# Optimization experiments

Hardware: AMD Instinct MI355X
Metric: run time of the kernel (lower is better)

Reference implementation:

```python
import jax, jax.numpy as jnp
import numpy as np

N_NODES = 100000
N_EDGES = 1600000
HIDDEN = 64


def setup_inputs() -> dict:
    key = jax.random.key(0)
    ks = jax.random.split(key, 10)
    s = 0.1
    x = jax.random.normal(ks[0], (N_NODES, 1), dtype=jnp.float32)
    edge_index = jax.random.randint(ks[1], (2, N_EDGES), 0, N_NODES, dtype=jnp.int32)
    edge_weight = jnp.ones((N_EDGES,), dtype=jnp.float32)
    f32 = jnp.float32
    return {
        "x": x,
        "edge_weight": edge_weight,
        "Wz": jax.random.normal(ks[2], (1, HIDDEN), f32) * s,
        "bz": jnp.zeros((HIDDEN,), f32),
        "Lz": jax.random.normal(ks[3], (2 * HIDDEN, HIDDEN), f32) * s,
        "lbz": jnp.zeros((HIDDEN,), f32),
        "Wr": jax.random.normal(ks[4], (1, HIDDEN), f32) * s,
        "br": jnp.zeros((HIDDEN,), f32),
        "Lr": jax.random.normal(ks[5], (2 * HIDDEN, HIDDEN), f32) * s,
        "lbr": jnp.zeros((HIDDEN,), f32),
        "Wh": jax.random.normal(ks[6], (1, HIDDEN), f32) * s,
        "bh": jnp.zeros((HIDDEN,), f32),
        "Lh": jax.random.normal(ks[7], (2 * HIDDEN, HIDDEN), f32) * s,
        "lbh": jnp.zeros((HIDDEN,), f32),
        "Wout": jax.random.normal(ks[8], (HIDDEN, 1), f32) * s,
        "bout": jnp.zeros((1,), f32),
        "edge_index": edge_index,
    }


def reference(x, edge_weight, Wz, bz, Lz, lbz, Wr, br, Lr, lbr,
              Wh, bh, Lh, lbh, Wout, bout, edge_index):
    N = x.shape[0]
    hidden = Wz.shape[1]
    src, dst = edge_index[0], edge_index[1]
    # GCN normalization with added self-loops (PyG gcn_norm)
    loop = jnp.arange(N, dtype=src.dtype)
    src2 = jnp.concatenate([src, loop])
    dst2 = jnp.concatenate([dst, loop])
    ew2 = jnp.concatenate([edge_weight, jnp.ones((N,), x.dtype)])
    deg = jax.ops.segment_sum(ew2, dst2, num_segments=N)  # [N]
    dinv = jnp.where(deg > 0, jax.lax.rsqrt(deg), 0.0)
    norm = dinv[src2] * ew2 * dinv[dst2]  # [E+N]

    def gcn(W, b):
        xw = x @ W  # [N, H]
        agg = jax.ops.segment_sum(xw[src2] * norm[:, None], dst2, num_segments=N)
        return agg + b

    # TGCN cell with H0 = 0 (no hidden state passed)
    H = jnp.zeros((N, hidden), x.dtype)
    Z = jax.nn.sigmoid(jnp.concatenate([gcn(Wz, bz), H], axis=1) @ Lz + lbz)
    R = jax.nn.sigmoid(jnp.concatenate([gcn(Wr, br), H], axis=1) @ Lr + lbr)
    Ht = jnp.tanh(jnp.concatenate([gcn(Wh, bh), H * R], axis=1) @ Lh + lbh)
    Hn = Z * H + (1.0 - Z) * Ht
    h = jax.nn.relu(Hn)
    return h @ Wout + bout
```

## Files before the change

kernel.cpp:

```cpp
#include <hip/hip_runtime.h>
#include <math.h>

#define HIDDEN 64
#define RANGE 16384
#define RSHIFT 14
#define G 32
#define PACK_SHIFT 17

__device__ __forceinline__ void map_rc(int b, int nranges, int& r, int& c) {
    int x = b & 7;
    int rest = b >> 3;
    r = rest % nranges;
    c = x + 8 * (rest / nranges);
}

__global__ __launch_bounds__(1024)
void k_binA(const int* __restrict__ dst, const int* __restrict__ src,
            const float* __restrict__ ew, float* __restrict__ partials,
            uint2* __restrict__ comp, int* __restrict__ counts,
            int N, int E, int nranges, int cap) {
    __shared__ float bins[RANGE];
    __shared__ int cursor;
    float4* b4 = (float4*)bins;
    for (int i = threadIdx.x; i < RANGE / 4; i += blockDim.x)
        b4[i] = make_float4(0.f, 0.f, 0.f, 0.f);
    if (threadIdx.x == 0) cursor = 0;
    __syncthreads();

    int r, c;
    map_rc(blockIdx.x, nranges, r, c);
    const int base = r * RANGE;
    const unsigned rsize = (unsigned)min(RANGE, N - base);
    uint2* slice = comp + (size_t)(r * G + c) * cap;

    long long e0 = (((long long)E * c) / G) & ~3LL;
    long long e1 = (c == G - 1) ? (long long)E
                                : ((((long long)E * (c + 1)) / G) & ~3LL);
    const int nvec = (int)((e1 - e0) >> 2);
    const int4*   dst4 = (const int4*)(dst + e0);
    const int4*   src4 = (const int4*)(src + e0);
    const float4* ew4  = (const float4*)(ew + e0);
    const int lane = threadIdx.x & 63;

    for (int i = threadIdx.x; i < nvec; i += blockDim.x) {
        int4   d = dst4[i];
        int4   s = src4[i];
        float4 t = ew4[i];
        int   dd[4] = {d.x, d.y, d.z, d.w};
        int   ss[4] = {s.x, s.y, s.z, s.w};
        float tt[4] = {t.x, t.y, t.z, t.w};
        #pragma unroll
        for (int j = 0; j < 4; ++j) {
            unsigned l = (unsigned)(dd[j] - base);
            bool p = l < rsize;
            if (p) atomicAdd(&bins[l], tt[j]);
            unsigned long long m = __ballot(p);
            if (m) {
                int leader = __ffsll((unsigned long long)m) - 1;
                int pre = __popcll(m & ((1ULL << lane) - 1ULL));
                int bpos = 0;
                if (lane == leader) bpos = atomicAdd(&cursor, __popcll(m));
                bpos = __shfl(bpos, leader);
                if (p) slice[bpos + pre] =
                    make_uint2((l << PACK_SHIFT) | (unsigned)ss[j],
                               __float_as_uint(tt[j]));
            }
        }
    }
    for (long long e = e0 + ((long long)nvec << 2) + threadIdx.x; e < e1; e += blockDim.x) {
        unsigned l = (unsigned)(dst[e] - base);
        if (l < rsize) {
            atomicAdd(&bins[l], ew[e]);
            int bpos = atomicAdd(&cursor, 1);
            slice[bpos] = make_uint2((l << PACK_SHIFT) | (unsigned)src[e],
                                     __float_as_uint(ew[e]));
        }
    }
    __syncthreads();

    float4* outp = (float4*)(partials + ((size_t)c * nranges + r) * RANGE);
    for (int i = threadIdx.x; i < RANGE / 4; i += blockDim.x) outp[i] = b4[i];
    if (threadIdx.x == 0) counts[r * G + c] = cursor;
}

__global__ void k_node(const float* __restrict__ x, const float* __restrict__ partials,
                       float* __restrict__ dinv, float* __restrict__ w,
                       int N, int nranges,
                       const float* __restrict__ Wz, const float* __restrict__ bz,
                       const float* __restrict__ Lz, const float* __restrict__ lbz,
                       const float* __restrict__ Wh, const float* __restrict__ bh,
                       const float* __restrict__ Lh, const float* __restrict__ lbh,
                       float* __restrict__ coeff) {
    int i = blockIdx.x * blockDim.x + threadIdx.x;
    if (i < N) {
        int r = i >> RSHIFT, local = i & (RANGE - 1);
        const float* p = partials + (size_t)r * RANGE + local;
        float d = 1.0f;
        #pragma unroll
        for (int c = 0; c < G; ++c) d += p[(size_t)c * nranges * RANGE];
        float di = rsqrtf(d);
        dinv[i] = di;
        w[i] = di * x[i];
    }
    if (blockIdx.x == 0 && threadIdx.x < HIDDEN) {
        int j = threadIdx.x;
        float vz = 0.f, cz = 0.f, vh = 0.f, ch = 0.f;
        for (int k = 0; k < HIDDEN; ++k) {
            float lz = Lz[k * HIDDEN + j];
            float lh = Lh[k * HIDDEN + j];
            vz += Wz[k] * lz;
            cz += bz[k] * lz;
            vh += Wh[k] * lh;
            ch += bh[k] * lh;
        }
        coeff[j]       = vz;
        coeff[64 + j]  = cz + lbz[j];
        coeff[128 + j] = vh;
        coeff[192 + j] = ch + lbh[j];
    }
}

__global__ __launch_bounds__(1024)
void k_binB(const uint2* __restrict__ comp, const int* __restrict__ counts,
            const float* __restrict__ w, float* __restrict__ partials,
            int nranges, int cap) {
    __shared__ float bins[RANGE];
    float4* b4 = (float4*)bins;
    for (int i = threadIdx.x; i < RANGE / 4; i += blockDim.x)
        b4[i] = make_float4(0.f, 0.f, 0.f, 0.f);
    __syncthreads();

    int r, c;
    map_rc(blockIdx.x, nranges, r, c);
    const uint2* slice = comp + (size_t)(r * G + c) * cap;
    const int n = counts[r * G + c];

    for (int i = threadIdx.x; i < n; i += blockDim.x) {
        uint2 e = slice[i];
        float v = w[e.x & ((1u << PACK_SHIFT) - 1u)] * __uint_as_float(e.y);
        atomicAdd(&bins[e.x >> PACK_SHIFT], v);
    }
    __syncthreads();

    float4* outp = (float4*)(partials + ((size_t)c * nranges + r) * RANGE);
    for (int i = threadIdx.x; i < RANGE / 4; i += blockDim.x) outp[i] = b4[i];
}

__global__ void k_out(const float* __restrict__ partials, const float* __restrict__ dinv,
                      const float* __restrict__ w, const float* __restrict__ coeff,
                      const float* __restrict__ Wout, const float* __restrict__ bout,
                      float* __restrict__ out, int N, int nranges) {
    __shared__ float c[5 * HIDDEN];
    __shared__ float b0;
    if (threadIdx.x < 4 * HIDDEN) c[threadIdx.x] = coeff[threadIdx.x];
    if (threadIdx.x < HIDDEN) c[4 * HIDDEN + threadIdx.x] = Wout[threadIdx.x];
    if (threadIdx.x == 0) b0 = bout[0];
    __syncthreads();
    int i = blockIdx.x * blockDim.x + threadIdx.x;
    if (i < N) {
        int r = i >> RSHIFT, local = i & (RANGE - 1);
        const float* p = partials + (size_t)r * RANGE + local;
        float g = w[i];
        #pragma unroll
        for (int k = 0; k < G; ++k) g += p[(size_t)k * nranges * RANGE];
        float si = dinv[i] * g;
        float acc = b0;
        #pragma unroll
        for (int j = 0; j < HIDDEN; ++j) {
            float zp = fminf(fmaxf(si * c[j] + c[64 + j], -30.f), 30.f);
            float hp = fminf(fmaxf(si * c[128 + j] + c[192 + j], -15.f), 15.f);
            float a  = __expf(2.0f * hp);
            float t  = (a - 1.0f) / (a + 1.0f);
            float zn = 1.0f / (1.0f + __expf(zp));
            float hn = zn * t;
            hn = hn > 0.0f ? hn : 0.0f;
            acc = fmaf(hn, c[256 + j], acc);
        }
        out[i] = acc;
    }
}

extern "C" void kernel_launch(void* const* d_in, const int* in_sizes, int n_in,
                              void* d_out, int out_size, void* d_ws, size_t ws_size,
                              hipStream_t stream) {
    const float* x    = (const float*)d_in[0];
    const float* ew   = (const float*)d_in[1];
    const float* Wz   = (const float*)d_in[2];
    const float* bz   = (const float*)d_in[3];
    const float* Lz   = (const float*)d_in[4];
    const float* lbz  = (const float*)d_in[5];
    const float* Wh   = (const float*)d_in[10];
    const float* bh   = (const float*)d_in[11];
    const float* Lh   = (const float*)d_in[12];
    const float* lbh  = (const float*)d_in[13];
    const float* Wout = (const float*)d_in[14];
    const float* bout = (const float*)d_in[15];
    const int*   eidx = (const int*)d_in[16];

    const int N = in_sizes[0];
    const int E = in_sizes[1];
    const int* src = eidx;
    const int* dst = eidx + E;

    const int nranges = (N + RANGE - 1) / RANGE;
    const int cap = (((E + G - 1) / G) + 15) & ~3;

    float* partials = (float*)d_ws;
    uint2* comp     = (uint2*)(partials + (size_t)G * nranges * RANGE);
    float* dinv     = (float*)(comp + (size_t)nranges * G * cap);
    float* w        = dinv + N;
    float* coeff    = w + N;
    int*   counts   = (int*)(coeff + 4 * HIDDEN);

    const int TB = 256;
    const int grid_bin = nranges * G;

    k_binA<<<grid_bin, 1024, 0, stream>>>(dst, src, ew, partials, comp, counts,
                                          N, E, nranges, cap);
    k_node<<<(N + TB - 1) / TB, TB, 0, stream>>>(x, partials, dinv, w, N, nranges,
                                                 Wz, bz, Lz, lbz, Wh, bh, Lh, lbh, coeff);
    k_binB<<<grid_bin, 1024, 0, stream>>>(comp, counts, w, partials, nranges, cap);
    k_out<<<(N + TB - 1) / TB, TB, 0, stream>>>(partials, dinv, w, coeff, Wout, bout,
                                                (float*)d_out, N, nranges);
}
```

Before: 154.8 us.

## Replace redundant per-range edge scans with single-pass global bucket compaction

Before, each of nranges*G blocks read its whole edge chunk and kept only edges whose destination fell in its range, so every edge was read nranges times. A new compaction kernel reads the edges once, counts them per destination range, reserves space with global atomics and scatters packed edges into per-range buckets. Both the degree pass and the weighted aggregation pass then use a templated bin kernel over contiguous bucket slices. This adds an extra kernel launch and a memset, and the scatter writes are less coalesced.

```diff
diff --git a/kernel.cpp b/kernel.cpp
--- a/kernel.cpp
+++ b/kernel.cpp
@@ -5,42 +5,44 @@
 #define RANGE 16384
 #define RSHIFT 14
 #define G 32
+#define NB 256
+#define MAXR 8
 #define PACK_SHIFT 17
 
-__device__ __forceinline__ void map_rc(int b, int nranges, int& r, int& c) {
-    int x = b & 7;
-    int rest = b >> 3;
-    r = rest % nranges;
-    c = x + 8 * (rest / nranges);
-}
-
-__global__ __launch_bounds__(1024)
-void k_binA(const int* __restrict__ dst, const int* __restrict__ src,
-            const float* __restrict__ ew, float* __restrict__ partials,
-            uint2* __restrict__ comp, int* __restrict__ counts,
-            int N, int E, int nranges, int cap) {
-    __shared__ float bins[RANGE];
-    __shared__ int cursor;
-    float4* b4 = (float4*)bins;
-    for (int i = threadIdx.x; i < RANGE / 4; i += blockDim.x)
-        b4[i] = make_float4(0.f, 0.f, 0.f, 0.f);
-    if (threadIdx.x == 0) cursor = 0;
-    __syncthreads();
-
-    int r, c;
-    map_rc(blockIdx.x, nranges, r, c);
-    const int base = r * RANGE;
-    const unsigned rsize = (unsigned)min(RANGE, N - base);
-    uint2* slice = comp + (size_t)(r * G + c) * cap;
-
-    long long e0 = (((long long)E * c) / G) & ~3LL;
-    long long e1 = (c == G - 1) ? (long long)E
-                                : ((((long long)E * (c + 1)) / G) & ~3LL);
+__global__ __launch_bounds__(256)
+void k_compact(const int* __restrict__ dst, const int* __restrict__ src,
+               const float* __restrict__ ew, uint2* __restrict__ comp,
+               int* __restrict__ gcur, int E, int capE) {
+    __shared__ int hist[MAXR];
+    __shared__ int rbase[MAXR];
+    __shared__ int cur[MAXR];
+    if (threadIdx.x < MAXR) hist[threadIdx.x] = 0;
+    __syncthreads();
+
+    long long e0 = (((long long)E * blockIdx.x) / NB) & ~3LL;
+    long long e1 = (blockIdx.x == NB - 1) ? (long long)E
+                                          : ((((long long)E * (blockIdx.x + 1)) / NB) & ~3LL);
     const int nvec = (int)((e1 - e0) >> 2);
     const int4*   dst4 = (const int4*)(dst + e0);
     const int4*   src4 = (const int4*)(src + e0);
     const float4* ew4  = (const float4*)(ew + e0);
-    const int lane = threadIdx.x & 63;
+
+    for (int i = threadIdx.x; i < nvec; i += blockDim.x) {
+        int4 d = dst4[i];
+        atomicAdd(&hist[d.x >> RSHIFT], 1);
+        atomicAdd(&hist[d.y >> RSHIFT], 1);
+        atomicAdd(&hist[d.z >> RSHIFT], 1);
+        atomicAdd(&hist[d.w >> RSHIFT], 1);
+    }
+    for (long long e = e0 + ((long long)nvec << 2) + threadIdx.x; e < e1; e += blockDim.x)
+        atomicAdd(&hist[dst[e] >> RSHIFT], 1);
+    __syncthreads();
+
+    if (threadIdx.x < MAXR) {
+        rbase[threadIdx.x] = atomicAdd(&gcur[threadIdx.x], hist[threadIdx.x]);
+        cur[threadIdx.x] = 0;
+    }
+    __syncthreads();
 
     for (int i = threadIdx.x; i < nvec; i += blockDim.x) {
         int4   d = dst4[i];
@@ -51,36 +53,50 @@
         float tt[4] = {t.x, t.y, t.z, t.w};
         #pragma unroll
         for (int j = 0; j < 4; ++j) {
-            unsigned l = (unsigned)(dd[j] - base);
-            bool p = l < rsize;
-            if (p) atomicAdd(&bins[l], tt[j]);
-            unsigned long long m = __ballot(p);
-            if (m) {
-                int leader = __ffsll((unsigned long long)m) - 1;
-                int pre = __popcll(m & ((1ULL << lane) - 1ULL));
-                int bpos = 0;
-                if (lane == leader) bpos = atomicAdd(&cursor, __popcll(m));
-                bpos = __shfl(bpos, leader);
-                if (p) slice[bpos + pre] =
-                    make_uint2((l << PACK_SHIFT) | (unsigned)ss[j],
-                               __float_as_uint(tt[j]));
-            }
+            int r = dd[j] >> RSHIFT;
+            int pos = atomicAdd(&cur[r], 1);
+            comp[(size_t)r * capE + rbase[r] + pos] =
+                make_uint2(((unsigned)(dd[j] & (RANGE - 1)) << PACK_SHIFT) | (unsigned)ss[j],
+                           __float_as_uint(tt[j]));
         }
     }
     for (long long e = e0 + ((long long)nvec << 2) + threadIdx.x; e < e1; e += blockDim.x) {
-        unsigned l = (unsigned)(dst[e] - base);
-        if (l < rsize) {
-            atomicAdd(&bins[l], ew[e]);
-            int bpos = atomicAdd(&cursor, 1);
-            slice[bpos] = make_uint2((l << PACK_SHIFT) | (unsigned)src[e],
-                                     __float_as_uint(ew[e]));
-        }
+        int d = dst[e];
+        int r = d >> RSHIFT;
+        int pos = atomicAdd(&cur[r], 1);
+        comp[(size_t)r * capE + rbase[r] + pos] =
+            make_uint2(((unsigned)(d & (RANGE - 1)) << PACK_SHIFT) | (unsigned)src[e],
+                       __float_as_uint(ew[e]));
+    }
+}
+
+template <bool WEIGHTED>
+__global__ __launch_bounds__(1024)
+void k_bin(const uint2* __restrict__ comp, const int* __restrict__ gcur,
+           const float* __restrict__ w, float* __restrict__ partials,
+           int nranges, int capE) {
+    __shared__ float bins[RANGE];
+    float4* b4 = (float4*)bins;
+    for (int i = threadIdx.x; i < RANGE / 4; i += blockDim.x)
+        b4[i] = make_float4(0.f, 0.f, 0.f, 0.f);
+    __syncthreads();
+
+    const int r = blockIdx.x / G, c = blockIdx.x % G;
+    const int len = gcur[r];
+    const uint2* bucket = comp + (size_t)r * capE;
+    const int a0 = (int)((long long)len * c / G);
+    const int a1 = (int)((long long)len * (c + 1) / G);
+
+    for (int i = a0 + threadIdx.x; i < a1; i += blockDim.x) {
+        uint2 e = bucket[i];
+        float v = __uint_as_float(e.y);
+        if (WEIGHTED) v *= w[e.x & ((1u << PACK_SHIFT) - 1u)];
+        atomicAdd(&bins[e.x >> PACK_SHIFT], v);
     }
     __syncthreads();
 
     float4* outp = (float4*)(partials + ((size_t)c * nranges + r) * RANGE);
     for (int i = threadIdx.x; i < RANGE / 4; i += blockDim.x) outp[i] = b4[i];
-    if (threadIdx.x == 0) counts[r * G + c] = cursor;
 }
 
 __global__ void k_node(const float* __restrict__ x, const float* __restrict__ partials,
@@ -118,32 +134,6 @@
         coeff[128 + j] = vh;
         coeff[192 + j] = ch + lbh[j];
     }
-}
-
-__global__ __launch_bounds__(1024)
-void k_binB(const uint2* __restrict__ comp, const int* __restrict__ counts,
-            const float* __restrict__ w, float* __restrict__ partials,
-            int nranges, int cap) {
-    __shared__ float bins[RANGE];
-    float4* b4 = (float4*)bins;
-    for (int i = threadIdx.x; i < RANGE / 4; i += blockDim.x)
-        b4[i] = make_float4(0.f, 0.f, 0.f, 0.f);
-    __syncthreads();
-
-    int r, c;
-    map_rc(blockIdx.x, nranges, r, c);
-    const uint2* slice = comp + (size_t)(r * G + c) * cap;
-    const int n = counts[r * G + c];
-
-    for (int i = threadIdx.x; i < n; i += blockDim.x) {
-        uint2 e = slice[i];
-        float v = w[e.x & ((1u << PACK_SHIFT) - 1u)] * __uint_as_float(e.y);
-        atomicAdd(&bins[e.x >> PACK_SHIFT], v);
-    }
-    __syncthreads();
-
-    float4* outp = (float4*)(partials + ((size_t)c * nranges + r) * RANGE);
-    for (int i = threadIdx.x; i < RANGE / 4; i += blockDim.x) outp[i] = b4[i];
 }
 
 __global__ void k_out(const float* __restrict__ partials, const float* __restrict__ dinv,
@@ -203,23 +193,25 @@
     const int* dst = eidx + E;
 
     const int nranges = (N + RANGE - 1) / RANGE;
-    const int cap = (((E + G - 1) / G) + 15) & ~3;
+    const int capE = E;
 
     float* partials = (float*)d_ws;
     uint2* comp     = (uint2*)(partials + (size_t)G * nranges * RANGE);
-    float* dinv     = (float*)(comp + (size_t)nranges * G * cap);
+    float* dinv     = (float*)(comp + (size_t)nranges * capE);
     float* w        = dinv + N;
     float* coeff    = w + N;
-    int*   counts   = (int*)(coeff + 4 * HIDDEN);
+    int*   gcur     = (int*)(coeff + 4 * HIDDEN);
 
     const int TB = 256;
     const int grid_bin = nranges * G;
 
-    k_binA<<<grid_bin, 1024, 0, stream>>>(dst, src, ew, partials, comp, counts,
-                                          N, E, nranges, cap);
+    hipMemsetAsync(gcur, 0, MAXR * sizeof(int), stream);
+    k_compact<<<NB, 256, 0, stream>>>(dst, src, ew, comp, gcur, E, capE);
+    k_bin<false><<<grid_bin, 1024, 0, stream>>>(comp, gcur, (const float*)nullptr,
+                                                partials, nranges, capE);
     k_node<<<(N + TB - 1) / TB, TB, 0, stream>>>(x, partials, dinv, w, N, nranges,
                                                  Wz, bz, Lz, lbz, Wh, bh, Lh, lbh, coeff);
-    k_binB<<<grid_bin, 1024, 0, stream>>>(comp, counts, w, partials, nranges, cap);
+    k_bin<true><<<grid_bin, 1024, 0, stream>>>(comp, gcur, w, partials, nranges, capE);
     k_out<<<(N + TB - 1) / TB, TB, 0, stream>>>(partials, dinv, w, coeff, Wout, bout,
                                                 (float*)d_out, N, nranges);
 }
```

New measurement: 158.1 us, median of 2. 1.02x slower.
